# Optimization experiments

Hardware: AMD Instinct MI355X
Metric: run time of the kernel (lower is better)

The kernel has to match this reference:

```python
import jax, jax.numpy as jnp
import numpy as np

B, S, D, H, HD = 2, 4096, 768, 12, 64
W = 256  # one-sided attention window (attention_window=512 // 2)
SCALE = 1.0 / np.sqrt(HD).astype(np.float32)
NEG = -1e9


def setup_inputs() -> dict:
    key = jax.random.key(0)
    ks = jax.random.split(key, 13)
    inp = {"hidden_states": jax.random.normal(ks[0], (B, S, D), dtype=jnp.float32)}
    names = ["Wq", "Wk", "Wv", "Wqg", "Wkg", "Wvg"]
    for i, n in enumerate(names):
        inp[n] = jax.random.normal(ks[1 + i], (D, D), dtype=jnp.float32) * 0.02
        inp["b" + n[1:]] = jax.random.normal(ks[7 + i], (D,), dtype=jnp.float32) * 0.02
    inp["num_global"] = 32
    return inp


def _heads(x):
    # [B,S,D] -> [B,H,S,HD]
    return x.reshape(B, S, H, HD).transpose(0, 2, 1, 3)


def longformer_attn(hidden_states, Wq, bq, Wk, bk, Wv, bv, Wqg, bqg, Wkg, bkg, Wvg, bvg, G):
    q = _heads(hidden_states @ Wq + bq) * SCALE
    k = _heads(hidden_states @ Wk + bk)
    v = _heads(hidden_states @ Wv + bv)

    nc = S // W  # number of query chunks
    # --- banded (sliding window) scores via overlapping key chunks of size 3W ---
    Qc = q.reshape(B, H, nc, W, HD)
    kpad = jnp.pad(k, ((0, 0), (0, 0), (W, W), (0, 0)))
    win_idx = jnp.arange(nc)[:, None] * W + jnp.arange(3 * W)[None, :]  # [nc, 3W]
    K3 = kpad[:, :, win_idx]  # [B,H,nc,3W,HD]
    band = jnp.einsum('bhcqd,bhckd->bhcqk', Qc, K3)  # [B,H,nc,W,3W]
    # mask: key abs position in range, and relative offset within [-W, W]
    c = jnp.arange(nc)[:, None, None]
    pq = jnp.arange(W)[None, :, None]
    e = jnp.arange(3 * W)[None, None, :]
    kabs = c * W + e - W
    valid = (kabs >= 0) & (kabs < S) & (e >= pq) & (e <= pq + 2 * W)
    band = jnp.where(valid[None, None], band, NEG).reshape(B, H, S, 3 * W)

    # --- all queries also attend to the G global keys (regular key proj) ---
    sg = jnp.einsum('bhsd,bhgd->bhsg', q, k[:, :, :G])  # [B,H,S,G]
    probs = jax.nn.softmax(jnp.concatenate([sg, band], axis=-1), axis=-1)
    pg, pb = probs[..., :G], probs[..., G:].reshape(B, H, nc, W, 3 * W)

    vpad = jnp.pad(v, ((0, 0), (0, 0), (W, W), (0, 0)))
    V3 = vpad[:, :, win_idx]  # [B,H,nc,3W,HD]
    out = jnp.einsum('bhcqk,bhckd->bhcqd', pb, V3).reshape(B, H, S, HD)
    out = out + jnp.einsum('bhsg,bhgd->bhsd', pg, v[:, :, :G])

    # --- global queries attend to ALL tokens with the *_global projections ---
    qg = _heads(hidden_states @ Wqg + bqg)[:, :, :G] * SCALE  # [B,H,G,HD]
    kgf = _heads(hidden_states @ Wkg + bkg)
    vgf = _heads(hidden_states @ Wvg + bvg)
    gp = jax.nn.softmax(jnp.einsum('bhgd,bhsd->bhgs', qg, kgf), axis=-1)
    gout = jnp.einsum('bhgs,bhsd->bhgd', gp, vgf)  # [B,H,G,HD]
    out = out.at[:, :, :G].set(gout)

    return out.transpose(0, 2, 1, 3).reshape(B, S, D)


def reference(hidden_states, Wq, bq, Wk, bk, Wv, bv, Wqg, bqg, Wkg, bkg, Wvg, bvg, num_global):
    return longformer_attn(hidden_states, Wq, bq, Wk, bk, Wv, bv, Wqg, bqg, Wkg, bkg, Wvg, bvg, int(num_global))
```

## Files before the change

kernel.cpp:

```cpp
#include <hip/hip_runtime.h>
#include <hip/hip_bf16.h>


#define DEVI __device__ __forceinline__
typedef _Float16 f16;
typedef _Float16 h4 __attribute__((ext_vector_type(4)));
typedef _Float16 f16x8 __attribute__((ext_vector_type(8)));
typedef __attribute__((ext_vector_type(4))) float float4v;

DEVI float4v mfma16(f16x8 a, f16x8 b, float4v c) {
    return __builtin_amdgcn_mfma_f32_16x16x32_f16(a, b, c, 0, 0, 0);
}

DEVI void gl_lds16(const f16* g, f16* l) {
    __builtin_amdgcn_global_load_lds(
        (const __attribute__((address_space(1))) unsigned int*)g,
        (__attribute__((address_space(3))) unsigned int*)l, 16, 0, 0);
}

__global__ __launch_bounds__(256) void prep(
    const float* __restrict__ x,
    const float* __restrict__ w0, const float* __restrict__ w1,
    const float* __restrict__ w2, const float* __restrict__ w3,
    const float* __restrict__ w4, const float* __restrict__ w5,
    f16* __restrict__ xh, f16* __restrict__ wt) {
    __shared__ float tile[64][65];
    int bid = blockIdx.x;
    if (bid < 6144) {
        int i = (bid * 256 + threadIdx.x) * 4;
        float4 v = *(const float4*)&x[i];
        h4 o = {(f16)v.x, (f16)v.y, (f16)v.z, (f16)v.w};
        *(h4*)&xh[i] = o;
    } else {
        int t = bid - 6144;
        int i = t / 144, rem = t - i * 144;
        int n0 = (rem % 12) * 64, k0 = (rem / 12) * 64;
        const float* W = (i == 0) ? w0 : (i == 1) ? w1 : (i == 2) ? w2
                       : (i == 3) ? w3 : (i == 4) ? w4 : w5;
        int tx = threadIdx.x & 63, ty = threadIdx.x >> 6;
#pragma unroll
        for (int yy = 0; yy < 64; yy += 4)
            tile[yy + ty][tx] = W[(size_t)(k0 + yy + ty) * 768 + n0 + tx];
        __syncthreads();
#pragma unroll
        for (int yy = 0; yy < 64; yy += 4)
            wt[(size_t)(i * 768 + n0 + yy + ty) * 768 + k0 + tx] = (f16)tile[tx][yy + ty];
    }
}

__global__ __launch_bounds__(256) void qkv_mfma4(
    const f16* __restrict__ Xh, const f16* __restrict__ Wt,
    const float* __restrict__ b0, const float* __restrict__ b1,
    const float* __restrict__ b2, const float* __restrict__ b3,
    const float* __restrict__ b4, const float* __restrict__ b5,
    f16* __restrict__ q, f16* __restrict__ k, f16* __restrict__ vT,
    f16* __restrict__ qg, f16* __restrict__ kg, f16* __restrict__ vgT) {
    constexpr int CLD = 136;
    __shared__ __align__(16) char smem[128 * CLD * 2];
    f16* At = (f16*)smem;
    f16* Bt = (f16*)(smem + 8192);
    f16* Cl = (f16*)smem;
    int tid = threadIdx.x, lane = tid & 63, wid = tid >> 6;
    int quad = lane >> 4, l15 = lane & 15;
    int m0 = blockIdx.x * 128;
    int grp = blockIdx.y / 6;
    if (grp == 3 && (m0 & 4095) != 0) return;
    int wm = (wid >> 1) * 64, wn = (wid & 1) * 64;
    const f16* arow0 = Xh + (size_t)m0 * 768;
    const f16* brow0 = Wt + (size_t)blockIdx.y * 128 * 768;

    float4v acc[4][4];
#pragma unroll
    for (int mt = 0; mt < 4; ++mt)
#pragma unroll
        for (int nt = 0; nt < 4; ++nt) acc[mt][nt] = (float4v){0.f, 0.f, 0.f, 0.f};

    int s0 = tid, s1 = tid + 256;
    int r0 = s0 >> 2, o0 = (s0 & 3) * 8;
    int r1 = s1 >> 2, o1 = (s1 & 3) * 8;
    f16* ldsA0 = &At[wid * 512];
    f16* ldsB0 = &Bt[wid * 512];
    f16* ldsA1 = &At[2048 + wid * 512];
    f16* ldsB1 = &Bt[2048 + wid * 512];
    for (int kt = 0; kt < 24; ++kt) {
        int k0 = kt * 32;
        __syncthreads();
        gl_lds16(&arow0[(size_t)r0 * 768 + k0 + o0], ldsA0);
        gl_lds16(&brow0[(size_t)r0 * 768 + k0 + o0], ldsB0);
        gl_lds16(&arow0[(size_t)r1 * 768 + k0 + o1], ldsA1);
        gl_lds16(&brow0[(size_t)r1 * 768 + k0 + o1], ldsB1);
        __syncthreads();
        f16x8 af[4], bf[4];
#pragma unroll
        for (int mt = 0; mt < 4; ++mt)
            af[mt] = *(const f16x8*)&At[(wm + mt * 16 + l15) * 32 + quad * 8];
#pragma unroll
        for (int nt = 0; nt < 4; ++nt)
            bf[nt] = *(const f16x8*)&Bt[(wn + nt * 16 + l15) * 32 + quad * 8];
#pragma unroll
        for (int mt = 0; mt < 4; ++mt)
#pragma unroll
            for (int nt = 0; nt < 4; ++nt) acc[mt][nt] = mfma16(af[mt], bf[nt], acc[mt][nt]);
    }
    __syncthreads();

    const float* Bsel = (grp == 0) ? b0 : (grp == 1) ? b1 : (grp == 2) ? b2
                      : (grp == 3) ? b3 : (grp == 4) ? b4 : b5;
    int nb = (blockIdx.y - grp * 6) * 128;
    int b = m0 >> 12;
    bool tr = (grp == 2 || grp == 5);

    if (tr) {
#pragma unroll
        for (int nt = 0; nt < 4; ++nt) {
            float bias = Bsel[nb + wn + nt * 16 + l15];
#pragma unroll
            for (int mt = 0; mt < 4; ++mt) {
                float4v a = acc[mt][nt];
                h4 pk = {(f16)(a[0] + bias), (f16)(a[1] + bias),
                         (f16)(a[2] + bias), (f16)(a[3] + bias)};
                *(h4*)&Cl[(wn + nt * 16 + l15) * CLD + wm + mt * 16 + quad * 4] = pk;
            }
        }
    } else {
        float scale = (grp == 0 || grp == 3) ? 0.125f : 1.0f;
#pragma unroll
        for (int nt = 0; nt < 4; ++nt) {
            float bias = Bsel[nb + wn + nt * 16 + l15];
#pragma unroll
            for (int mt = 0; mt < 4; ++mt) {
                float4v a = acc[mt][nt];
#pragma unroll
                for (int r = 0; r < 4; ++r)
                    Cl[(wm + mt * 16 + quad * 4 + r) * CLD + wn + nt * 16 + l15] =
                        (f16)((a[r] + bias) * scale);
            }
        }
    }
    __syncthreads();

    if (tr) {
        f16* base = (grp == 2) ? vT : vgT;
        int c = tid & 127, sh = (tid >> 7) * 64;
        int ncol = nb + c, h = ncol >> 6, hd = ncol & 63;
        f16* dst = &base[((size_t)((b * 12 + h) * 64 + hd)) * 4096 + (m0 & 4095) + sh];
        const f16* src = &Cl[c * CLD + sh];
#pragma unroll
        for (int i = 0; i < 8; ++i)
            *(f16x8*)&dst[i * 8] = *(const f16x8*)&src[i * 8];
    } else {
        int sl = tid & 127, hh = tid >> 7;
        int s = (m0 & 4095) + sl;
        int h = (nb + hh * 64) >> 6;
        const f16* src = &Cl[sl * CLD + hh * 64];
        f16* dst = nullptr;
        if (grp == 3) {
            if (s < 32) dst = &qg[((size_t)((b * 12 + h) * 32 + s)) * 64];
        } else {
            f16* baseb = (grp == 0) ? q : (grp == 1) ? k : kg;
            dst = &baseb[((size_t)((b * 12 + h) * 4096 + s)) * 64];
        }
        if (dst)
#pragma unroll
            for (int i = 0; i < 8; ++i)
                *(f16x8*)&dst[i * 8] = *(const f16x8*)&src[i * 8];
    }
}

__global__ __launch_bounds__(256, 3) void band_mfma5(
    const f16* __restrict__ q, const f16* __restrict__ k, const f16* __restrict__ vT,
    float* __restrict__ out) {
    constexpr int LDK = 72, LDV = 136, LDP = 40;
    __shared__ __align__(16) f16 Kt[128 * LDK];
    __shared__ __align__(16) f16 Vt[64 * LDV];
    __shared__ __align__(16) f16 Pt[4][32 * LDP];
    int tid = threadIdx.x, lane = tid & 63, wid = tid >> 6;
    int quad = lane >> 4, l15 = lane & 15;
    int c = blockIdx.x & 31, h = (blockIdx.x >> 5) % 12, b = blockIdx.x / 384;
    const f16* qsl = q + (size_t)(b * 12 + h) * 4096 * 64;
    const f16* ksl = k + (size_t)(b * 12 + h) * 4096 * 64;
    const f16* vsl = vT + (size_t)(b * 12 + h) * 64 * 4096;
    int q0 = c * 128;
    int pq0 = q0 + wid * 32;

    f16x8 qf[2][2];
#pragma unroll
    for (int qg = 0; qg < 2; ++qg)
#pragma unroll
        for (int ks = 0; ks < 2; ++ks)
            qf[qg][ks] = *(const f16x8*)&qsl[(size_t)(pq0 + qg * 16 + l15) * 64 +
                                             ks * 32 + quad * 8];

    float4v Ot[4][2];
#pragma unroll
    for (int dt = 0; dt < 4; ++dt)
#pragma unroll
        for (int qg = 0; qg < 2; ++qg) Ot[dt][qg] = (float4v){0.f, 0.f, 0.f, 0.f};
    float lacc[2] = {0.f, 0.f};
    f16* PW = &Pt[wid][0];

    {
#pragma unroll
        for (int jt = 0; jt < 2; ++jt) {
            f16x8 kf0 = *(const f16x8*)&ksl[(size_t)(jt * 16 + l15) * 64 + quad * 8];
            f16x8 kf1 = *(const f16x8*)&ksl[(size_t)(jt * 16 + l15) * 64 + 32 + quad * 8];
#pragma unroll
            for (int qg = 0; qg < 2; ++qg) {
                float4v sacc = (float4v){0.f, 0.f, 0.f, 0.f};
                sacc = mfma16(kf0, qf[qg][0], sacc);
                sacc = mfma16(kf1, qf[qg][1], sacc);
                float p0 = __expf(sacc[0]), p1 = __expf(sacc[1]);
                float p2 = __expf(sacc[2]), p3 = __expf(sacc[3]);
                lacc[qg] += (p0 + p1) + (p2 + p3);
                h4 pk = {(f16)p0, (f16)p1, (f16)p2, (f16)p3};
                *(h4*)&PW[(qg * 16 + l15) * LDP + jt * 16 + quad * 4] = pk;
            }
        }
        f16x8 pf0 = *(const f16x8*)&PW[l15 * LDP + quad * 8];
        f16x8 pf1 = *(const f16x8*)&PW[(16 + l15) * LDP + quad * 8];
#pragma unroll
        for (int dt = 0; dt < 4; ++dt) {
            f16x8 vf = *(const f16x8*)&vsl[(size_t)(dt * 16 + l15) * 4096 + quad * 8];
            Ot[dt][0] = mfma16(vf, pf0, Ot[dt][0]);
            Ot[dt][1] = mfma16(vf, pf1, Ot[dt][1]);
        }
    }

    for (int r = 0; r < 5; ++r) {
        int kb = q0 - 256 + r * 128;
        if (kb < 0 || kb >= 4096) continue;
        __syncthreads();
        {
            int kr = tid >> 1, ko = (tid & 1) * 32;
            const f16* ks2 = &ksl[(size_t)(kb + kr) * 64 + ko];
            f16* kd = &Kt[kr * LDK + ko];
#pragma unroll
            for (int i = 0; i < 4; ++i) *(f16x8*)&kd[i * 8] = *(const f16x8*)&ks2[i * 8];
            int vr = tid >> 2, vo = (tid & 3) * 32;
            const f16* vs2 = &vsl[(size_t)vr * 4096 + kb + vo];
            f16* vd = &Vt[vr * LDV + vo];
#pragma unroll
            for (int i = 0; i < 4; ++i) *(f16x8*)&vd[i * 8] = *(const f16x8*)&vs2[i * 8];
        }
        __syncthreads();

        if (kb + 127 < pq0 - 256 || kb > pq0 + 287) continue;

#pragma unroll
        for (int tt = 0; tt < 2; ++tt) {
            int tb = kb + tt * 64;
            if (tb + 63 < pq0 - 256 || tb > pq0 + 287) continue;
#pragma unroll
            for (int hf = 0; hf < 2; ++hf) {
#pragma unroll
                for (int jt = 0; jt < 2; ++jt) {
                    int jl = tt * 64 + hf * 32 + jt * 16;
                    f16x8 kf0 = *(const f16x8*)&Kt[(jl + l15) * LDK + quad * 8];
                    f16x8 kf1 = *(const f16x8*)&Kt[(jl + l15) * LDK + 32 + quad * 8];
                    int j0 = kb + jl;
#pragma unroll
                    for (int qg = 0; qg < 2; ++qg) {
                        int qlo = pq0 + qg * 16;
                        h4 pk = {(f16)0.f, (f16)0.f, (f16)0.f, (f16)0.f};
                        bool dead = (j0 < qlo - 271) || (j0 > qlo + 271);
                        if (!dead) {
                            float4v sacc = (float4v){0.f, 0.f, 0.f, 0.f};
                            sacc = mfma16(kf0, qf[qg][0], sacc);
                            sacc = mfma16(kf1, qf[qg][1], sacc);
                            float p[4];
                            bool full = (j0 >= qlo - 241) && (j0 <= qlo + 241);
                            if (full) {
#pragma unroll
                                for (int rr = 0; rr < 4; ++rr) p[rr] = __expf(sacc[rr]);
                            } else {
#pragma unroll
                                for (int rr = 0; rr < 4; ++rr) {
                                    int d = (j0 + quad * 4 + rr) - (qlo + l15);
                                    p[rr] = ((unsigned)(d + 256) <= 512u) ? __expf(sacc[rr]) : 0.f;
                                }
                            }
                            lacc[qg] += (p[0] + p[1]) + (p[2] + p[3]);
                            pk = (h4){(f16)p[0], (f16)p[1], (f16)p[2], (f16)p[3]};
                        }
                        *(h4*)&PW[(qg * 16 + l15) * LDP + jt * 16 + quad * 4] = pk;
                    }
                }
                f16x8 pf0 = *(const f16x8*)&PW[l15 * LDP + quad * 8];
                f16x8 pf1 = *(const f16x8*)&PW[(16 + l15) * LDP + quad * 8];
#pragma unroll
                for (int dt = 0; dt < 4; ++dt) {
                    f16x8 vf = *(const f16x8*)&Vt[(dt * 16 + l15) * LDV +
                                                  tt * 64 + hf * 32 + quad * 8];
                    Ot[dt][0] = mfma16(vf, pf0, Ot[dt][0]);
                    Ot[dt][1] = mfma16(vf, pf1, Ot[dt][1]);
                }
            }
        }
    }

#pragma unroll
    for (int qg = 0; qg < 2; ++qg) {
        float lsum = lacc[qg];
        lsum += __shfl_xor(lsum, 16);
        lsum += __shfl_xor(lsum, 32);
        float inv = 1.f / lsum;
        size_t orow = (size_t)(b * 4096 + pq0 + qg * 16 + l15) * 768 + h * 64;
#pragma unroll
        for (int dt = 0; dt < 4; ++dt) {
            float4 o4 = {Ot[dt][qg][0] * inv, Ot[dt][qg][1] * inv,
                         Ot[dt][qg][2] * inv, Ot[dt][qg][3] * inv};
            *(float4*)&out[orow + dt * 16 + quad * 4] = o4;
        }
    }
}

__global__ __launch_bounds__(256) void global_part(
    const f16* __restrict__ qg, const f16* __restrict__ kg, const f16* __restrict__ vgT,
    float* __restrict__ Opart, float* __restrict__ Lpart) {
    constexpr int LDP = 72;
    __shared__ __align__(16) f16 Pt[4][32 * LDP];
    __shared__ __align__(16) float Osh[4][64 * 32];
    __shared__ float Lsh[4][32];
    int tid = threadIdx.x, lane = tid & 63, wid = tid >> 6;
    int quad = lane >> 4, l15 = lane & 15;
    int sl = blockIdx.x & 7, bh = blockIdx.x >> 3;
    const f16* qsl = qg + (size_t)bh * 32 * 64;
    const f16* ksl = kg + (size_t)bh * 4096 * 64;
    const f16* vsl = vgT + (size_t)bh * 64 * 4096;
    int kbase = sl * 512 + wid * 128;

    f16x8 qf[2][2];
#pragma unroll
    for (int g = 0; g < 2; ++g)
#pragma unroll
        for (int ks = 0; ks < 2; ++ks)
            qf[g][ks] = *(const f16x8*)&qsl[(size_t)(g * 16 + l15) * 64 + ks * 32 + quad * 8];

    float4v Ot[4][2];
#pragma unroll
    for (int dt = 0; dt < 4; ++dt)
#pragma unroll
        for (int g = 0; g < 2; ++g) Ot[dt][g] = (float4v){0.f, 0.f, 0.f, 0.f};
    float lacc[2] = {0.f, 0.f};
    f16* PW = &Pt[wid][0];

#pragma unroll
    for (int hf = 0; hf < 2; ++hf) {
        int kh0 = kbase + hf * 64;
#pragma unroll
        for (int kt = 0; kt < 4; ++kt) {
            int jb = kh0 + kt * 16;
            f16x8 kf0 = *(const f16x8*)&ksl[(size_t)(jb + l15) * 64 + quad * 8];
            f16x8 kf1 = *(const f16x8*)&ksl[(size_t)(jb + l15) * 64 + 32 + quad * 8];
#pragma unroll
            for (int g = 0; g < 2; ++g) {
                float4v sacc = (float4v){0.f, 0.f, 0.f, 0.f};
                sacc = mfma16(kf0, qf[g][0], sacc);
                sacc = mfma16(kf1, qf[g][1], sacc);
                float p0 = __expf(sacc[0]), p1 = __expf(sacc[1]);
                float p2 = __expf(sacc[2]), p3 = __expf(sacc[3]);
                lacc[g] += (p0 + p1) + (p2 + p3);
                h4 pk = {(f16)p0, (f16)p1, (f16)p2, (f16)p3};
                *(h4*)&PW[(g * 16 + l15) * LDP + kt * 16 + quad * 4] = pk;
            }
        }
#pragma unroll
        for (int kh = 0; kh < 2; ++kh) {
            f16x8 pf0 = *(const f16x8*)&PW[l15 * LDP + kh * 32 + quad * 8];
            f16x8 pf1 = *(const f16x8*)&PW[(16 + l15) * LDP + kh * 32 + quad * 8];
#pragma unroll
            for (int dt = 0; dt < 4; ++dt) {
                f16x8 vf = *(const f16x8*)&vsl[(size_t)(dt * 16 + l15) * 4096 +
                                               kh0 + kh * 32 + quad * 8];
                Ot[dt][0] = mfma16(vf, pf0, Ot[dt][0]);
                Ot[dt][1] = mfma16(vf, pf1, Ot[dt][1]);
            }
        }
    }

#pragma unroll
    for (int g = 0; g < 2; ++g) {
        lacc[g] += __shfl_xor(lacc[g], 16);
        lacc[g] += __shfl_xor(lacc[g], 32);
    }
    if (quad == 0) { Lsh[wid][l15] = lacc[0]; Lsh[wid][16 + l15] = lacc[1]; }
#pragma unroll
    for (int dt = 0; dt < 4; ++dt)
#pragma unroll
        for (int g = 0; g < 2; ++g)
#pragma unroll
            for (int r = 0; r < 4; ++r)
                Osh[wid][(dt * 16 + quad * 4 + r) * 32 + g * 16 + l15] = Ot[dt][g][r];
    __syncthreads();
#pragma unroll
    for (int i = 0; i < 8; ++i) {
        int idx = tid + i * 256;
        int d = idx & 63, qq = idx >> 6;
        float v = Osh[0][d * 32 + qq] + Osh[1][d * 32 + qq] +
                  Osh[2][d * 32 + qq] + Osh[3][d * 32 + qq];
        Opart[(size_t)blockIdx.x * 2048 + idx] = v;
    }
    if (tid < 32)
        Lpart[blockIdx.x * 32 + tid] = Lsh[0][tid] + Lsh[1][tid] + Lsh[2][tid] + Lsh[3][tid];
}

__global__ __launch_bounds__(256) void global_reduce(
    const float* __restrict__ Opart, const float* __restrict__ Lpart,
    float* __restrict__ out) {
    __shared__ float Ls[32];
    int tid = threadIdx.x, bh = blockIdx.x;
    int b = bh / 12, h = bh % 12;
    if (tid < 32) {
        float s = 0.f;
#pragma unroll
        for (int sl = 0; sl < 8; ++sl) s += Lpart[(bh * 8 + sl) * 32 + tid];
        Ls[tid] = s;
    }
    __syncthreads();
#pragma unroll
    for (int i = 0; i < 8; ++i) {
        int idx = tid + i * 256;
        int d = idx & 63, qq = idx >> 6;
        float o = 0.f;
#pragma unroll
        for (int sl = 0; sl < 8; ++sl) o += Opart[(size_t)(bh * 8 + sl) * 2048 + idx];
        out[(size_t)(b * 4096 + qq) * 768 + h * 64 + d] = o / Ls[qq];
    }
}

extern "C" void kernel_launch(void* const* d_in, const int* in_sizes, int n_in,
                              void* d_out, int out_size, void* d_ws, size_t ws_size,
                              hipStream_t stream) {
    const float* hs = (const float*)d_in[0];
    float* outp = (float*)d_out;

    char* p = (char*)d_ws;
    const size_t SLAB = (size_t)2 * 12 * 4096 * 64 * sizeof(f16);
    f16* qb   = (f16*)(p + 0 * SLAB);
    f16* kb   = (f16*)(p + 1 * SLAB);
    f16* vtb  = (f16*)(p + 2 * SLAB);
    f16* kgb  = (f16*)(p + 3 * SLAB);
    f16* vgtb = (f16*)(p + 4 * SLAB);
    f16* qgb  = (f16*)(p + 5 * SLAB);
    char* p2  = p + 5 * SLAB + 196608;
    f16* xh   = (f16*)p2;
    f16* wt   = (f16*)(p2 + SLAB);
    char* p3  = p2 + SLAB + 7077888;
    float* Opart = (float*)p3;
    float* Lpart = (float*)(p3 + 1572864);

    prep<<<7008, 256, 0, stream>>>(
        hs,
        (const float*)d_in[1], (const float*)d_in[3], (const float*)d_in[5],
        (const float*)d_in[7], (const float*)d_in[9], (const float*)d_in[11],
        xh, wt);
    qkv_mfma4<<<dim3(64, 36), 256, 0, stream>>>(
        xh, wt,
        (const float*)d_in[2], (const float*)d_in[4], (const float*)d_in[6],
        (const float*)d_in[8], (const float*)d_in[10], (const float*)d_in[12],
        qb, kb, vtb, qgb, kgb, vgtb);
    band_mfma5<<<768, 256, 0, stream>>>(qb, kb, vtb, outp);
    global_part<<<192, 256, 0, stream>>>(qgb, kgb, vgtb, Opart, Lpart);
    global_reduce<<<24, 256, 0, stream>>>(Opart, Lpart, outp);
}
```

Measured before the change: 232.9 us.

## Double-buffer QKV GEMM LDS tiles and XOR-swizzle to avoid bank conflicts

The QKV projection GEMM now keeps two LDS buffers for A and B tiles, so the global-to-LDS load of the next k-step is issued before the MFMAs on the current one, and each iteration needs one barrier instead of two. The column offset inside each 32-wide tile row is XOR-swizzled by row, on both the store and the fragment reads, to spread LDS accesses across banks. This hides load latency behind compute. The risk is that correctness depends on the async global_load_lds writes completing before the barrier that follows them.

```diff
diff --git a/kernel.cpp b/kernel.cpp
--- a/kernel.cpp
+++ b/kernel.cpp
@@ -48,7 +48,7 @@
     }
 }
 
-__global__ __launch_bounds__(256) void qkv_mfma4(
+__global__ __launch_bounds__(256) void qkv_mfma5(
     const f16* __restrict__ Xh, const f16* __restrict__ Wt,
     const float* __restrict__ b0, const float* __restrict__ b1,
     const float* __restrict__ b2, const float* __restrict__ b3,
@@ -57,8 +57,10 @@
     f16* __restrict__ qg, f16* __restrict__ kg, f16* __restrict__ vgT) {
     constexpr int CLD = 136;
     __shared__ __align__(16) char smem[128 * CLD * 2];
-    f16* At = (f16*)smem;
-    f16* Bt = (f16*)(smem + 8192);
+    f16* At0 = (f16*)smem;
+    f16* Bt0 = (f16*)(smem + 8192);
+    f16* At1 = (f16*)(smem + 16384);
+    f16* Bt1 = (f16*)(smem + 24576);
     f16* Cl = (f16*)smem;
     int tid = threadIdx.x, lane = tid & 63, wid = tid >> 6;
     int quad = lane >> 4, l15 = lane & 15;
@@ -76,33 +78,40 @@
         for (int nt = 0; nt < 4; ++nt) acc[mt][nt] = (float4v){0.f, 0.f, 0.f, 0.f};
 
     int s0 = tid, s1 = tid + 256;
-    int r0 = s0 >> 2, o0 = (s0 & 3) * 8;
-    int r1 = s1 >> 2, o1 = (s1 & 3) * 8;
-    f16* ldsA0 = &At[wid * 512];
-    f16* ldsB0 = &Bt[wid * 512];
-    f16* ldsA1 = &At[2048 + wid * 512];
-    f16* ldsB1 = &Bt[2048 + wid * 512];
+    int r0 = s0 >> 2, r1 = s1 >> 2;
+    int o0 = (((s0 & 3) ^ ((r0 >> 1) & 3)) << 3);
+    int o1 = (((s1 & 3) ^ ((r1 >> 1) & 3)) << 3);
+    int sw8 = ((quad ^ ((l15 >> 1) & 3)) << 3);
+
+    auto STAGE = [&](int kt, f16* A, f16* B) {
+        int k0 = kt << 5;
+        gl_lds16(&arow0[(size_t)r0 * 768 + k0 + o0], A + wid * 512);
+        gl_lds16(&brow0[(size_t)r0 * 768 + k0 + o0], B + wid * 512);
+        gl_lds16(&arow0[(size_t)r1 * 768 + k0 + o1], A + 2048 + wid * 512);
+        gl_lds16(&brow0[(size_t)r1 * 768 + k0 + o1], B + 2048 + wid * 512);
+    };
+
+    f16* Ac = At0; f16* Bc = Bt0; f16* An = At1; f16* Bn = Bt1;
+    STAGE(0, Ac, Bc);
+    __syncthreads();
     for (int kt = 0; kt < 24; ++kt) {
-        int k0 = kt * 32;
+        if (kt < 23) STAGE(kt + 1, An, Bn);
+        f16x8 af[4], bf[4];
+#pragma unroll
+        for (int mt = 0; mt < 4; ++mt)
+            af[mt] = *(const f16x8*)&Ac[(wm + mt * 16 + l15) * 32 + sw8];
+#pragma unroll
+        for (int nt = 0; nt < 4; ++nt)
+            bf[nt] = *(const f16x8*)&Bc[(wn + nt * 16 + l15) * 32 + sw8];
+#pragma unroll
+        for (int mt = 0; mt < 4; ++mt)
+#pragma unroll
+            for (int nt = 0; nt < 4; ++nt) acc[mt][nt] = mfma16(af[mt], bf[nt], acc[mt][nt]);
         __syncthreads();
-        gl_lds16(&arow0[(size_t)r0 * 768 + k0 + o0], ldsA0);
-        gl_lds16(&brow0[(size_t)r0 * 768 + k0 + o0], ldsB0);
-        gl_lds16(&arow0[(size_t)r1 * 768 + k0 + o1], ldsA1);
-        gl_lds16(&brow0[(size_t)r1 * 768 + k0 + o1], ldsB1);
-        __syncthreads();
-        f16x8 af[4], bf[4];
-#pragma unroll
-        for (int mt = 0; mt < 4; ++mt)
-            af[mt] = *(const f16x8*)&At[(wm + mt * 16 + l15) * 32 + quad * 8];
-#pragma unroll
-        for (int nt = 0; nt < 4; ++nt)
-            bf[nt] = *(const f16x8*)&Bt[(wn + nt * 16 + l15) * 32 + quad * 8];
-#pragma unroll
-        for (int mt = 0; mt < 4; ++mt)
-#pragma unroll
-            for (int nt = 0; nt < 4; ++nt) acc[mt][nt] = mfma16(af[mt], bf[nt], acc[mt][nt]);
-    }
-    __syncthreads();
+        f16* t;
+        t = Ac; Ac = An; An = t;
+        t = Bc; Bc = Bn; Bn = t;
+    }
 
     const float* Bsel = (grp == 0) ? b0 : (grp == 1) ? b1 : (grp == 2) ? b2
                       : (grp == 3) ? b3 : (grp == 4) ? b4 : b5;
@@ -454,7 +463,7 @@
         (const float*)d_in[1], (const float*)d_in[3], (const float*)d_in[5],
         (const float*)d_in[7], (const float*)d_in[9], (const float*)d_in[11],
         xh, wt);
-    qkv_mfma4<<<dim3(64, 36), 256, 0, stream>>>(
+    qkv_mfma5<<<dim3(64, 36), 256, 0, stream>>>(
         xh, wt,
         (const float*)d_in[2], (const float*)d_in[4], (const float*)d_in[6],
         (const float*)d_in[8], (const float*)d_in[10], (const float*)d_in[12],
```

Result: no change. 235.6 us (+1.2%).

## Rewrite QKV projection GEMM with 256x256 tiles and 4-stage async LDS pipeline

Applied to the files above, without the earlier changes.

Replaces the 128x128-tile, 256-thread projection GEMM with a 256x256-tile, 512-thread kernel. It uses a four-buffer global-to-LDS prefetch pipeline with explicit vmcnt waits and a single barrier per k-step, an XOR-swizzled LDS layout to avoid bank conflicts, and raised wave priority around the MFMA bursts. The aim is to hide global load latency and cut barrier and LDS overhead, while larger tiles raise data reuse. In exchange the grid has far fewer blocks and uses more LDS and registers per block, which may limit occupancy or leave CUs idle.

```diff
diff --git a/kernel.cpp b/kernel.cpp
--- a/kernel.cpp
+++ b/kernel.cpp
@@ -48,91 +48,144 @@
     }
 }
 
-__global__ __launch_bounds__(256) void qkv_mfma4(
+__global__ __launch_bounds__(512, 2) void qkv_mfma7(
     const f16* __restrict__ Xh, const f16* __restrict__ Wt,
     const float* __restrict__ b0, const float* __restrict__ b1,
     const float* __restrict__ b2, const float* __restrict__ b3,
     const float* __restrict__ b4, const float* __restrict__ b5,
     f16* __restrict__ q, f16* __restrict__ k, f16* __restrict__ vT,
     f16* __restrict__ qg, f16* __restrict__ kg, f16* __restrict__ vgT) {
-    constexpr int CLD = 136;
-    __shared__ __align__(16) char smem[128 * CLD * 2];
-    f16* At = (f16*)smem;
-    f16* Bt = (f16*)(smem + 8192);
+    constexpr int CLD = 264;
+    __shared__ __align__(16) char smem[256 * CLD * 2];
+    f16* As = (f16*)smem;
+    f16* Bs = (f16*)(smem + 65536);
     f16* Cl = (f16*)smem;
+
     int tid = threadIdx.x, lane = tid & 63, wid = tid >> 6;
     int quad = lane >> 4, l15 = lane & 15;
-    int m0 = blockIdx.x * 128;
-    int grp = blockIdx.y / 6;
+    int wr = wid >> 2, wc = wid & 3;
+    int m0 = blockIdx.x * 256;
+    int grp = blockIdx.y / 3;
     if (grp == 3 && (m0 & 4095) != 0) return;
-    int wm = (wid >> 1) * 64, wn = (wid & 1) * 64;
+    int nb = (blockIdx.y - grp * 3) * 256;
     const f16* arow0 = Xh + (size_t)m0 * 768;
-    const f16* brow0 = Wt + (size_t)blockIdx.y * 128 * 768;
-
-    float4v acc[4][4];
-#pragma unroll
-    for (int mt = 0; mt < 4; ++mt)
+    const f16* brow0 = Wt + (size_t)(grp * 768 + nb) * 768;
+
+    int rS = tid >> 2;
+    int cgS = (((tid & 3) ^ ((rS >> 1) & 3)) << 3);
+    int sw8 = ((quad ^ ((l15 >> 1) & 3)) << 3);
+    f16* Asw = As + wid * 512;
+    f16* Bsw = Bs + wid * 512;
+    int wrb = wr * 128;
+    int wcb = wc * 64;
+
+    float4v acc[8][4];
+#pragma unroll
+    for (int mt = 0; mt < 8; ++mt)
 #pragma unroll
         for (int nt = 0; nt < 4; ++nt) acc[mt][nt] = (float4v){0.f, 0.f, 0.f, 0.f};
 
-    int s0 = tid, s1 = tid + 256;
-    int r0 = s0 >> 2, o0 = (s0 & 3) * 8;
-    int r1 = s1 >> 2, o1 = (s1 & 3) * 8;
-    f16* ldsA0 = &At[wid * 512];
-    f16* ldsB0 = &Bt[wid * 512];
-    f16* ldsA1 = &At[2048 + wid * 512];
-    f16* ldsB1 = &Bt[2048 + wid * 512];
-    for (int kt = 0; kt < 24; ++kt) {
-        int k0 = kt * 32;
-        __syncthreads();
-        gl_lds16(&arow0[(size_t)r0 * 768 + k0 + o0], ldsA0);
-        gl_lds16(&brow0[(size_t)r0 * 768 + k0 + o0], ldsB0);
-        gl_lds16(&arow0[(size_t)r1 * 768 + k0 + o1], ldsA1);
-        gl_lds16(&brow0[(size_t)r1 * 768 + k0 + o1], ldsB1);
-        __syncthreads();
-        f16x8 af[4], bf[4];
-#pragma unroll
-        for (int mt = 0; mt < 4; ++mt)
-            af[mt] = *(const f16x8*)&At[(wm + mt * 16 + l15) * 32 + quad * 8];
-#pragma unroll
-        for (int nt = 0; nt < 4; ++nt)
-            bf[nt] = *(const f16x8*)&Bt[(wn + nt * 16 + l15) * 32 + quad * 8];
-#pragma unroll
-        for (int mt = 0; mt < 4; ++mt)
-#pragma unroll
-            for (int nt = 0; nt < 4; ++nt) acc[mt][nt] = mfma16(af[mt], bf[nt], acc[mt][nt]);
-    }
+#define STAGE_T(K0, SBUF)                                                      \
+    do {                                                                       \
+        gl_lds16(&arow0[(size_t)rS * 768 + (K0) + cgS], Asw + (SBUF) * 8192);  \
+        gl_lds16(&arow0[(size_t)(128 + rS) * 768 + (K0) + cgS],                \
+                 Asw + (SBUF) * 8192 + 4096);                                  \
+        gl_lds16(&brow0[(size_t)rS * 768 + (K0) + cgS], Bsw + (SBUF) * 8192);  \
+        gl_lds16(&brow0[(size_t)(128 + rS) * 768 + (K0) + cgS],                \
+                 Bsw + (SBUF) * 8192 + 4096);                                  \
+    } while (0)
+
+#define TILE(K3, BUF, SBUF, WN, DOSTG)                                         \
+    do {                                                                       \
+        asm volatile("s_waitcnt vmcnt(" #WN ")" ::: "memory");                 \
+        __builtin_amdgcn_s_barrier();                                          \
+        __builtin_amdgcn_sched_barrier(0);                                     \
+        const f16* Ab = As + (BUF) * 8192;                                     \
+        const f16* Bb = Bs + (BUF) * 8192;                                     \
+        if (DOSTG) {                                                           \
+            gl_lds16(&arow0[(size_t)rS * 768 + (K3) + cgS],                    \
+                     Asw + (SBUF) * 8192);                                     \
+            gl_lds16(&arow0[(size_t)(128 + rS) * 768 + (K3) + cgS],            \
+                     Asw + (SBUF) * 8192 + 4096);                              \
+        }                                                                      \
+        f16x8 bfv[4];                                                          \
+        _Pragma("unroll") for (int j = 0; j < 4; ++j)                          \
+            bfv[j] = *(const f16x8*)&Bb[(wcb + j * 16 + l15) * 32 + sw8];      \
+        {                                                                      \
+            f16x8 af[4];                                                       \
+            _Pragma("unroll") for (int i = 0; i < 4; ++i)                      \
+                af[i] = *(const f16x8*)&Ab[(wrb + i * 16 + l15) * 32 + sw8];   \
+            __builtin_amdgcn_s_setprio(1);                                     \
+            _Pragma("unroll") for (int i = 0; i < 4; ++i)                      \
+                _Pragma("unroll") for (int j = 0; j < 4; ++j)                  \
+                    acc[i][j] = mfma16(af[i], bfv[j], acc[i][j]);              \
+            __builtin_amdgcn_s_setprio(0);                                     \
+        }                                                                      \
+        if (DOSTG) {                                                           \
+            gl_lds16(&brow0[(size_t)rS * 768 + (K3) + cgS],                    \
+                     Bsw + (SBUF) * 8192);                                     \
+            gl_lds16(&brow0[(size_t)(128 + rS) * 768 + (K3) + cgS],            \
+                     Bsw + (SBUF) * 8192 + 4096);                              \
+        }                                                                      \
+        {                                                                      \
+            f16x8 af[4];                                                       \
+            _Pragma("unroll") for (int i = 0; i < 4; ++i)                      \
+                af[i] = *(const f16x8*)&Ab[(wrb + 64 + i * 16 + l15) * 32 + sw8]; \
+            __builtin_amdgcn_s_setprio(1);                                     \
+            _Pragma("unroll") for (int i = 0; i < 4; ++i)                      \
+                _Pragma("unroll") for (int j = 0; j < 4; ++j)                  \
+                    acc[4 + i][j] = mfma16(af[i], bfv[j], acc[4 + i][j]);      \
+            __builtin_amdgcn_s_setprio(0);                                     \
+        }                                                                      \
+    } while (0)
+
+    STAGE_T(0, 0);
+    STAGE_T(32, 1);
+    STAGE_T(64, 2);
+    for (int m = 0; m < 5; ++m) {
+        int kb = m * 128;
+        TILE(kb + 96, 0, 3, 8, true);
+        TILE(kb + 128, 1, 0, 8, true);
+        TILE(kb + 160, 2, 1, 8, true);
+        TILE(kb + 192, 3, 2, 8, true);
+    }
+    TILE(736, 0, 3, 8, true);
+    TILE(0, 1, 0, 8, false);
+    TILE(0, 2, 0, 4, false);
+    TILE(0, 3, 0, 0, false);
+#undef TILE
+#undef STAGE_T
+
     __syncthreads();
 
     const float* Bsel = (grp == 0) ? b0 : (grp == 1) ? b1 : (grp == 2) ? b2
                       : (grp == 3) ? b3 : (grp == 4) ? b4 : b5;
-    int nb = (blockIdx.y - grp * 6) * 128;
     int b = m0 >> 12;
     bool tr = (grp == 2 || grp == 5);
 
     if (tr) {
 #pragma unroll
         for (int nt = 0; nt < 4; ++nt) {
-            float bias = Bsel[nb + wn + nt * 16 + l15];
-#pragma unroll
-            for (int mt = 0; mt < 4; ++mt) {
+            float bias = Bsel[nb + wcb + nt * 16 + l15];
+#pragma unroll
+            for (int mt = 0; mt < 8; ++mt) {
                 float4v a = acc[mt][nt];
                 h4 pk = {(f16)(a[0] + bias), (f16)(a[1] + bias),
                          (f16)(a[2] + bias), (f16)(a[3] + bias)};
-                *(h4*)&Cl[(wn + nt * 16 + l15) * CLD + wm + mt * 16 + quad * 4] = pk;
+                *(h4*)&Cl[(wcb + nt * 16 + l15) * CLD + wrb + mt * 16 + quad * 4] = pk;
             }
         }
     } else {
         float scale = (grp == 0 || grp == 3) ? 0.125f : 1.0f;
 #pragma unroll
         for (int nt = 0; nt < 4; ++nt) {
-            float bias = Bsel[nb + wn + nt * 16 + l15];
-#pragma unroll
-            for (int mt = 0; mt < 4; ++mt) {
+            float bias = Bsel[nb + wcb + nt * 16 + l15];
+#pragma unroll
+            for (int mt = 0; mt < 8; ++mt) {
                 float4v a = acc[mt][nt];
 #pragma unroll
                 for (int r = 0; r < 4; ++r)
-                    Cl[(wm + mt * 16 + quad * 4 + r) * CLD + wn + nt * 16 + l15] =
+                    Cl[(wrb + mt * 16 + quad * 4 + r) * CLD + wcb + nt * 16 + l15] =
                         (f16)((a[r] + bias) * scale);
             }
         }
@@ -141,29 +194,36 @@
 
     if (tr) {
         f16* base = (grp == 2) ? vT : vgT;
-        int c = tid & 127, sh = (tid >> 7) * 64;
-        int ncol = nb + c, h = ncol >> 6, hd = ncol & 63;
-        f16* dst = &base[((size_t)((b * 12 + h) * 64 + hd)) * 4096 + (m0 & 4095) + sh];
-        const f16* src = &Cl[c * CLD + sh];
-#pragma unroll
-        for (int i = 0; i < 8; ++i)
+        int nn = tid >> 1, hf = tid & 1;
+        int ncol = nb + nn, h = ncol >> 6, hd = ncol & 63;
+        const f16* src = &Cl[nn * CLD + hf * 128];
+        f16* dst = &base[((size_t)((b * 12 + h) * 64 + hd)) * 4096 + (m0 & 4095) + hf * 128];
+#pragma unroll
+        for (int i = 0; i < 16; ++i)
             *(f16x8*)&dst[i * 8] = *(const f16x8*)&src[i * 8];
     } else {
-        int sl = tid & 127, hh = tid >> 7;
-        int s = (m0 & 4095) + sl;
-        int h = (nb + hh * 64) >> 6;
-        const f16* src = &Cl[sl * CLD + hh * 64];
-        f16* dst = nullptr;
+        int rr = tid >> 1, hf = tid & 1;
+        int s = (m0 & 4095) + rr;
+        const f16* src = &Cl[rr * CLD + hf * 128];
+        int hb = nb >> 6;
         if (grp == 3) {
-            if (s < 32) dst = &qg[((size_t)((b * 12 + h) * 32 + s)) * 64];
+            if (s < 32) {
+#pragma unroll
+                for (int i = 0; i < 16; ++i) {
+                    int h = hb + hf * 2 + (i >> 3), hd = (i & 7) * 8;
+                    *(f16x8*)&qg[((size_t)((b * 12 + h) * 32 + s)) * 64 + hd] =
+                        *(const f16x8*)&src[i * 8];
+                }
+            }
         } else {
             f16* baseb = (grp == 0) ? q : (grp == 1) ? k : kg;
-            dst = &baseb[((size_t)((b * 12 + h) * 4096 + s)) * 64];
-        }
-        if (dst)
-#pragma unroll
-            for (int i = 0; i < 8; ++i)
-                *(f16x8*)&dst[i * 8] = *(const f16x8*)&src[i * 8];
+#pragma unroll
+            for (int i = 0; i < 16; ++i) {
+                int h = hb + hf * 2 + (i >> 3), hd = (i & 7) * 8;
+                *(f16x8*)&baseb[((size_t)((b * 12 + h) * 4096 + s)) * 64 + hd] =
+                    *(const f16x8*)&src[i * 8];
+            }
+        }
     }
 }
 
@@ -454,7 +514,7 @@
         (const float*)d_in[1], (const float*)d_in[3], (const float*)d_in[5],
         (const float*)d_in[7], (const float*)d_in[9], (const float*)d_in[11],
         xh, wt);
-    qkv_mfma4<<<dim3(64, 36), 256, 0, stream>>>(
+    qkv_mfma7<<<dim3(32, 18), 512, 0, stream>>>(
         xh, wt,
         (const float*)d_in[2], (const float*)d_in[4], (const float*)d_in[6],
         (const float*)d_in[8], (const float*)d_in[10], (const float*)d_in[12],
```

After: 230.9 us. No clear change (-0.8%).
